# Kernel tuning notes

Measured on AMD Instinct MI355X. Metric: run time of the kernel, lower is better.

The kernel has to match this reference:

```python
import jax, jax.numpy as jnp
import numpy as np

PAD_VALUE = float(np.finfo(np.float32).min)


def setup_inputs() -> dict:
    key = jax.random.key(0)
    k1, k2, k3 = jax.random.split(key, 3)
    T, B, L, P, Q = 512, 8, 64, 256, 128  # frames, batch, languages, shared phones, phonemes
    phone_logits = jax.random.normal(k1, (T, B, P), dtype=jnp.float32)
    language_ids = jax.random.randint(k2, (B,), 0, L, dtype=jnp.int32)
    # mimicking the blank/identity initialization in __init__.
    mat = (jax.random.uniform(k3, (L, P, Q)) < 0.05).astype(jnp.float32)
    diag = jnp.arange(Q)
    mat = mat.at[:, diag, diag].set(1.0)
    mask = mat == 0.0  # ~allophone_matrix.bool()
    return {
        "phone_logits": phone_logits,
        "language_ids": language_ids,
        "allophone_matrices": mat,
        "allophone_mask": mask,
    }


def reference(phone_logits, language_ids, allophone_matrices, allophone_mask):
    # Batched gather of per-language expert matrices (replaces the Python loop)
    mats = allophone_matrices[language_ids]   # [B, P, Q]
    masks = allophone_mask[language_ids]      # [B, P, Q] bool
    # logits[:, :, :, None] * matrix, masked_fill, max over shared-phone axis P
    scores = phone_logits[:, :, :, None] * mats[None]          # [T, B, P, Q]
    scores = jnp.where(masks[None], PAD_VALUE, scores)
    return scores.max(axis=2)                                  # [T, B, Q]
```

## Files before the change

kernel.cpp:

```cpp
#include <hip/hip_runtime.h>
#include <hip/hip_bf16.h>
#include <stdint.h>

#define T_DIM   512
#define B_DIM   8
#define P_DIM   256
#define Q_DIM   128
#define MAXC    48
#define NW4     (MAXC / 4)
#define TCHUNK  16


static __device__ __forceinline__ uint32_t bf16_rn(float x) {
    const uint32_t u = __float_as_uint(x);
    return (u + 0x7FFFu + ((u >> 16) & 1u)) >> 16;
}

__global__ __launch_bounds__(512, 1) void AllophoneMapping_kernel(
    const float* __restrict__ logits,
    const int*   __restrict__ lang_ids,
    const float* __restrict__ mats,
    float*       __restrict__ out)
{
    __shared__ uint32_t s_mask[8][Q_DIM];
    __shared__ uint32_t s_idx[NW4][Q_DIM];
    __shared__ uint32_t s_cnt[Q_DIM];
    __shared__ uint32_t s_pair[8][P_DIM];

    const int tid  = threadIdx.x;
    const int b    = blockIdx.x & (B_DIM - 1);
    const int t0   = (blockIdx.x >> 3) * TCHUNK;
    const int lang = lang_ids[b];
    const float* __restrict__ mat = mats + (size_t)lang * (P_DIM * Q_DIM);

    const int p    = tid & (P_DIM - 1);
    const int rgrp = tid >> 8;
    float v[8];
    #pragma unroll
    for (int r = 0; r < 8; ++r)
        v[r] = logits[((size_t)(t0 + rgrp * 8 + r) * B_DIM + b) * P_DIM + p];

    {
        const int w  = tid >> 6;
        const int q2 = (tid & 63) * 2;
        const float* __restrict__ base = mat + (size_t)(w * 32) * Q_DIM + q2;
        uint32_t b0 = 0, b1 = 0;
        #pragma unroll
        for (int i = 0; i < 32; ++i) {
            const float2 m2 = *reinterpret_cast<const float2*>(base + (size_t)i * Q_DIM);
            if (m2.x != 0.0f) b0 |= (1u << i);
            if (m2.y != 0.0f) b1 |= (1u << i);
        }
        s_mask[w][q2]     = b0;
        s_mask[w][q2 + 1] = b1;
    }

    #pragma unroll
    for (int j = 0; j < 4; ++j)
        s_pair[rgrp * 4 + j][p] = bf16_rn(v[2 * j]) | (bf16_rn(v[2 * j + 1]) << 16);
    __syncthreads();

    if (tid < Q_DIM) {
        const int q = tid;
        int cnt = 0;
        uint32_t acc = 0;
        #pragma unroll
        for (int w = 0; w < 8; ++w) {
            uint32_t bits = s_mask[w][q];
            while (bits) {
                const int i = __ffs(bits) - 1;
                bits &= bits - 1;
                if (cnt < MAXC) {
                    acc |= (uint32_t)(w * 32 + i) << (8 * (cnt & 3));
                    if ((cnt & 3) == 3) { s_idx[cnt >> 2][q] = acc; acc = 0; }
                }
                ++cnt;
            }
        }
        const int true_cnt = cnt < MAXC ? cnt : MAXC;
        while (cnt < MAXC && (cnt & 3) != 0) {
            acc |= (uint32_t)q << (8 * (cnt & 3));
            if ((cnt & 3) == 3) { s_idx[cnt >> 2][q] = acc; acc = 0; }
            ++cnt;
        }
        s_cnt[q] = (uint32_t)true_cnt;
    }
    __syncthreads();

    {
        const int q = tid & (Q_DIM - 1);
        const int h = tid >> 7;
        const uint32_t cnt = s_cnt[q];
        uint32_t wv[NW4];
        #pragma unroll
        for (int j = 0; j < NW4; ++j) wv[j] = s_idx[j][q];

        const uint32_t* __restrict__ pa = s_pair[2 * h];
        const uint32_t* __restrict__ pb = s_pair[2 * h + 1];

        const uint32_t d0 = pa[q], d1 = pb[q];
        float m0 = __uint_as_float(d0 << 16);
        float m1 = __uint_as_float(d0 & 0xFFFF0000u);
        float m2 = __uint_as_float(d1 << 16);
        float m3 = __uint_as_float(d1 & 0xFFFF0000u);

        #pragma unroll
        for (int j = 0; j < NW4; ++j) {
            if ((uint32_t)(4 * j) < cnt) {
                const uint32_t u = wv[j];
                #pragma unroll
                for (int k = 0; k < 4; ++k) {
                    const uint32_t pi = (u >> (8 * k)) & 255u;
                    const uint32_t g0 = pa[pi];
                    const uint32_t g1 = pb[pi];
                    m0 = fmaxf(m0, __uint_as_float(g0 << 16));
                    m1 = fmaxf(m1, __uint_as_float(g0 & 0xFFFF0000u));
                    m2 = fmaxf(m2, __uint_as_float(g1 << 16));
                    m3 = fmaxf(m3, __uint_as_float(g1 & 0xFFFF0000u));
                }
            }
        }

        float* __restrict__ o = out + ((size_t)(t0 + 4 * h) * B_DIM + b) * Q_DIM + q;
        o[0 * B_DIM * Q_DIM] = m0;
        o[1 * B_DIM * Q_DIM] = m1;
        o[2 * B_DIM * Q_DIM] = m2;
        o[3 * B_DIM * Q_DIM] = m3;
    }
}

extern "C" void kernel_launch(void* const* d_in, const int* in_sizes, int n_in,
                              void* d_out, int out_size, void* d_ws, size_t ws_size,
                              hipStream_t stream) {
    (void)in_sizes; (void)n_in; (void)d_ws; (void)ws_size; (void)out_size;
    const float* logits   = (const float*)d_in[0];
    const int*   lang_ids = (const int*)d_in[1];
    const float* mats     = (const float*)d_in[2];
    float* out = (float*)d_out;

    AllophoneMapping_kernel<<<dim3((T_DIM / TCHUNK) * B_DIM), dim3(512), 0, stream>>>(
        logits, lang_ids, mats, out);
}
```

Measured before the change: 14.73 us.

## Parallelize sparse index compaction across all threads with popcount prefix sums

Index-list construction used to run serially on 128 threads, each walking 256 mask bits. It is now split across all 512 threads: each thread handles 64 rows of the P axis, counts its set bits with popcount, takes an exclusive prefix over the four groups, and scatters byte indices into a byte-addressed shared buffer. The mask build also switches to float4 loads over half-columns. This targets the serial bottleneck between the two barriers, at the cost of an extra barrier inside a block, byte-granular shared stores, and a padding write done only by group 0.

```diff
diff --git a/kernel.cpp b/kernel.cpp
--- a/kernel.cpp
+++ b/kernel.cpp
@@ -22,8 +22,9 @@
     const float* __restrict__ mats,
     float*       __restrict__ out)
 {
-    __shared__ uint32_t s_mask[8][Q_DIM];
-    __shared__ uint32_t s_idx[NW4][Q_DIM];
+    __shared__ uint32_t s_maskh[2][8][Q_DIM];
+    __shared__ uint32_t s_psum[4][Q_DIM];
+    __shared__ uint8_t  s_idxb[NW4 * Q_DIM * 4];
     __shared__ uint32_t s_cnt[Q_DIM];
     __shared__ uint32_t s_pair[8][P_DIM];
 
@@ -41,18 +42,24 @@
         v[r] = logits[((size_t)(t0 + rgrp * 8 + r) * B_DIM + b) * P_DIM + p];
 
     {
-        const int w  = tid >> 6;
-        const int q2 = (tid & 63) * 2;
-        const float* __restrict__ base = mat + (size_t)(w * 32) * Q_DIM + q2;
-        uint32_t b0 = 0, b1 = 0;
+        const int ihalf = tid >> 8;
+        const int w     = (tid >> 5) & 7;
+        const int q4    = (tid & 31) * 4;
+        const float* __restrict__ base =
+            mat + (size_t)(w * 32 + ihalf * 16) * Q_DIM + q4;
+        uint32_t b0 = 0, b1 = 0, b2 = 0, b3 = 0;
         #pragma unroll
-        for (int i = 0; i < 32; ++i) {
-            const float2 m2 = *reinterpret_cast<const float2*>(base + (size_t)i * Q_DIM);
-            if (m2.x != 0.0f) b0 |= (1u << i);
-            if (m2.y != 0.0f) b1 |= (1u << i);
+        for (int k = 0; k < 16; ++k) {
+            const float4 m4 = *reinterpret_cast<const float4*>(base + (size_t)k * Q_DIM);
+            if (m4.x != 0.0f) b0 |= (1u << k);
+            if (m4.y != 0.0f) b1 |= (1u << k);
+            if (m4.z != 0.0f) b2 |= (1u << k);
+            if (m4.w != 0.0f) b3 |= (1u << k);
         }
-        s_mask[w][q2]     = b0;
-        s_mask[w][q2 + 1] = b1;
+        s_maskh[ihalf][w][q4]     = b0;
+        s_maskh[ihalf][w][q4 + 1] = b1;
+        s_maskh[ihalf][w][q4 + 2] = b2;
+        s_maskh[ihalf][w][q4 + 3] = b3;
     }
 
     #pragma unroll
@@ -60,30 +67,47 @@
         s_pair[rgrp * 4 + j][p] = bf16_rn(v[2 * j]) | (bf16_rn(v[2 * j + 1]) << 16);
     __syncthreads();
 
-    if (tid < Q_DIM) {
-        const int q = tid;
-        int cnt = 0;
-        uint32_t acc = 0;
+    {
+        const int g = tid >> 7;
+        const int q = tid & (Q_DIM - 1);
+        const uint32_t w0 = s_maskh[0][2 * g][q]     | (s_maskh[1][2 * g][q] << 16);
+        const uint32_t w1 = s_maskh[0][2 * g + 1][q] | (s_maskh[1][2 * g + 1][q] << 16);
+        s_psum[g][q] = (uint32_t)(__popc(w0) + __popc(w1));
+        __syncthreads();
+
+        int prefix = 0, total = 0;
         #pragma unroll
-        for (int w = 0; w < 8; ++w) {
-            uint32_t bits = s_mask[w][q];
-            while (bits) {
-                const int i = __ffs(bits) - 1;
-                bits &= bits - 1;
-                if (cnt < MAXC) {
-                    acc |= (uint32_t)(w * 32 + i) << (8 * (cnt & 3));
-                    if ((cnt & 3) == 3) { s_idx[cnt >> 2][q] = acc; acc = 0; }
-                }
-                ++cnt;
-            }
+        for (int gg = 0; gg < 4; ++gg) {
+            const int c = (int)s_psum[gg][q];
+            prefix += (gg < g) ? c : 0;
+            total  += c;
         }
-        const int true_cnt = cnt < MAXC ? cnt : MAXC;
-        while (cnt < MAXC && (cnt & 3) != 0) {
-            acc |= (uint32_t)q << (8 * (cnt & 3));
-            if ((cnt & 3) == 3) { s_idx[cnt >> 2][q] = acc; acc = 0; }
-            ++cnt;
+        const int cnt = total < MAXC ? total : MAXC;
+
+        int rank = prefix;
+        const int pbase = 2 * g * 32;
+        uint32_t bits = w0;
+        while (bits) {
+            const int i = __ffs(bits) - 1;
+            bits &= bits - 1;
+            if (rank < MAXC)
+                s_idxb[(rank >> 2) * (Q_DIM * 4) + q * 4 + (rank & 3)] = (uint8_t)(pbase + i);
+            ++rank;
         }
-        s_cnt[q] = (uint32_t)true_cnt;
+        bits = w1;
+        while (bits) {
+            const int i = __ffs(bits) - 1;
+            bits &= bits - 1;
+            if (rank < MAXC)
+                s_idxb[(rank >> 2) * (Q_DIM * 4) + q * 4 + (rank & 3)] = (uint8_t)(pbase + 32 + i);
+            ++rank;
+        }
+        if (g == 0) {
+            s_cnt[q] = (uint32_t)cnt;
+            const int cpad = (cnt + 3) & ~3;
+            for (int s = cnt; s < cpad; ++s)
+                s_idxb[(s >> 2) * (Q_DIM * 4) + q * 4 + (s & 3)] = (uint8_t)q;
+        }
     }
     __syncthreads();
 
@@ -93,7 +117,8 @@
         const uint32_t cnt = s_cnt[q];
         uint32_t wv[NW4];
         #pragma unroll
-        for (int j = 0; j < NW4; ++j) wv[j] = s_idx[j][q];
+        for (int j = 0; j < NW4; ++j)
+            wv[j] = *reinterpret_cast<const uint32_t*>(&s_idxb[j * (Q_DIM * 4) + q * 4]);
 
         const uint32_t* __restrict__ pa = s_pair[2 * h];
         const uint32_t* __restrict__ pb = s_pair[2 * h + 1];
```

After: 18.60 us. 26.2% more time.
